# Optimization experiments

Measured on AMD Instinct MI355X. Metric: run time of the kernel, lower is better.

The kernel has to match this reference:

```python
import jax, jax.numpy as jnp
import numpy as np

NHEAD = 8
TEMP = 1.0
LAMB = 1.0
G_MIN = 1e-3


def _linear(x, w, b):
    # torch nn.Linear convention: w is (out, in)
    return x @ w.T + b


def _ln(x, s, b):
    m = x.mean(-1, keepdims=True)
    v = ((x - m) ** 2).mean(-1, keepdims=True)
    return (x - m) / jnp.sqrt(v + 1e-5) * s + b


def _gate(x, w, b):
    # UncertaintyGate, gate_mode='mu_times_evi'
    nig = _linear(x, w, b)  # [B, L, 4]
    mu = nig[..., 0]
    v = jax.nn.softplus(nig[..., 1]) + 1e-6
    alpha = jax.nn.softplus(nig[..., 2]) + 1.0 + 1e-6
    beta = jax.nn.softplus(nig[..., 3]) + 1e-6
    sigma_e2 = beta / (v * (alpha - 1.0))
    g = jax.nn.sigmoid(mu) * jnp.exp(-LAMB * sigma_e2)
    return jnp.clip(g, G_MIN, 1.0)  # [B, L]


def _cross_attn(q, k, v, gate, mask):
    B, Lq, D = q.shape
    Lk = k.shape[1]
    hd = D // NHEAD
    q = q.reshape(B, Lq, NHEAD, hd).transpose(0, 2, 1, 3)
    k = k.reshape(B, Lk, NHEAD, hd).transpose(0, 2, 1, 3)
    v = v.reshape(B, Lk, NHEAD, hd).transpose(0, 2, 1, 3)
    scores = jnp.einsum('bhqd,bhkd->bhqk', q, k) / jnp.sqrt(jnp.float32(hd))
    scores = scores + jnp.log(gate + 1e-9)[:, None, None, :]  # per-key log-gate bias
    scores = jnp.where(mask[:, None, None, :] == 0, -1e9, scores)
    attn = jax.nn.softmax(scores / TEMP, axis=-1)
    out = jnp.einsum('bhqk,bhkd->bhqd', attn, v)
    return out.transpose(0, 2, 1, 3).reshape(B, Lq, D)


def _ffn(x, w1, b1, w2, b2):
    return _linear(jax.nn.gelu(_linear(x, w1, b1), approximate=False), w2, b2)


def setup_inputs() -> dict:
    key = jax.random.key(0)
    ks = iter(jax.random.split(key, 64))
    D, B, Ld, Lp = 512, 16, 256, 1024
    def w(shape, s=0.02):
        return jax.random.normal(next(ks), shape, jnp.float32) * s
    inp = {
        'h_d': jax.random.normal(next(ks), (B, Ld, D), jnp.float32),
        'h_p': jax.random.normal(next(ks), (B, Lp, D), jnp.float32),
        'gd_w': w((4, D)), 'gd_b': jnp.zeros((4,), jnp.float32),
        'gp_w': w((4, D)), 'gp_b': jnp.zeros((4,), jnp.float32),
        'wqd_w': w((D, D)), 'wqd_b': jnp.zeros((D,), jnp.float32),
        'wkp_w': w((D, D)), 'wkp_b': jnp.zeros((D,), jnp.float32),
        'wvp_w': w((D, D)), 'wvp_b': jnp.zeros((D,), jnp.float32),
        'wqp_w': w((D, D)), 'wqp_b': jnp.zeros((D,), jnp.float32),
        'wkd_w': w((D, D)), 'wkd_b': jnp.zeros((D,), jnp.float32),
        'wvd_w': w((D, D)), 'wvd_b': jnp.zeros((D,), jnp.float32),
        'od_w': w((D, D)), 'od_b': jnp.zeros((D,), jnp.float32),
        'op_w': w((D, D)), 'op_b': jnp.zeros((D,), jnp.float32),
        'fd1_w': w((4 * D, D)), 'fd1_b': jnp.zeros((4 * D,), jnp.float32),
        'fd2_w': w((D, 4 * D)), 'fd2_b': jnp.zeros((D,), jnp.float32),
        'fp1_w': w((4 * D, D)), 'fp1_b': jnp.zeros((4 * D,), jnp.float32),
        'fp2_w': w((D, 4 * D)), 'fp2_b': jnp.zeros((D,), jnp.float32),
        'nd1_s': jnp.ones((D,), jnp.float32), 'nd1_b': jnp.zeros((D,), jnp.float32),
        'nd2_s': jnp.ones((D,), jnp.float32), 'nd2_b': jnp.zeros((D,), jnp.float32),
        'np1_s': jnp.ones((D,), jnp.float32), 'np1_b': jnp.zeros((D,), jnp.float32),
        'np2_s': jnp.ones((D,), jnp.float32), 'np2_b': jnp.zeros((D,), jnp.float32),
        'mask_d': jnp.ones((B, Ld), jnp.int32),
        'mask_p': jnp.ones((B, Lp), jnp.int32),
    }
    return inp


def reference(h_d, h_p, gd_w, gd_b, gp_w, gp_b, wqd_w, wqd_b, wkp_w, wkp_b,
              wvp_w, wvp_b, wqp_w, wqp_b, wkd_w, wkd_b, wvd_w, wvd_b,
              od_w, od_b, op_w, op_b, fd1_w, fd1_b, fd2_w, fd2_b,
              fp1_w, fp1_b, fp2_w, fp2_b, nd1_s, nd1_b, nd2_s, nd2_b,
              np1_s, np1_b, np2_s, np2_b, mask_d, mask_p):
    # gates are computed from the ORIGINAL inputs
    g_d = _gate(h_d, gd_w, gd_b)
    g_p = _gate(h_p, gp_w, gp_b)
    # drug attends to protein
    attn_d = _cross_attn(_linear(h_d, wqd_w, wqd_b),
                         _linear(h_p, wkp_w, wkp_b),
                         _linear(h_p, wvp_w, wvp_b), g_p, mask_p)
    h_d = _ln(h_d + _linear(attn_d, od_w, od_b), nd1_s, nd1_b)
    # protein attends to UPDATED drug (matches original control flow)
    attn_p = _cross_attn(_linear(h_p, wqp_w, wqp_b),
                         _linear(h_d, wkd_w, wkd_b),
                         _linear(h_d, wvd_w, wvd_b), g_d, mask_d)
    h_p = _ln(h_p + _linear(attn_p, op_w, op_b), np1_s, np1_b)
    h_d = _ln(h_d + _ffn(h_d, fd1_w, fd1_b, fd2_w, fd2_b), nd2_s, nd2_b)
    h_p = _ln(h_p + _ffn(h_p, fp1_w, fp1_b, fp2_w, fp2_b), np2_s, np2_b)
    return (h_d, h_p)
```

## Files before the change

kernel.cpp:

```cpp
#include <hip/hip_runtime.h>

typedef float f32x4 __attribute__((ext_vector_type(4)));
typedef short bfrag __attribute__((ext_vector_type(8)));
typedef short s16x8 __attribute__((ext_vector_type(8)));
typedef unsigned short u16;

__device__ __forceinline__ u16 f2bf(float f) {
  union { float f; unsigned u; } x; x.f = f;
  unsigned r = x.u + 0x7fffu + ((x.u >> 16) & 1u);
  return (u16)(r >> 16);
}
__device__ __forceinline__ float bf2f(u16 v) {
  union { unsigned u; float f; } x; x.u = ((unsigned)v) << 16;
  return x.f;
}

__device__ __forceinline__ void g2l16(const void* g, void* l) {
  void* gnc = const_cast<void*>(g);
  __builtin_amdgcn_global_load_lds((__attribute__((address_space(1))) void*)gnc,
                                   (__attribute__((address_space(3))) void*)l, 16, 0, 0);
}

__device__ __forceinline__ f32x4 mfma16(bfrag a, bfrag b, f32x4 c) {
  asm volatile("v_mfma_f32_16x16x32_bf16 %0, %1, %2, %0" : "+v"(c) : "v"(a), "v"(b));
  return c;
}

__device__ __forceinline__ float wred_sum(float s) {
  #pragma unroll
  for (int o = 32; o; o >>= 1) s += __shfl_xor(s, o);
  return s;
}

struct CvtArgs {
  const float* s[14];
  u16* d[14];
  int eb[14];
};

__global__ __launch_bounds__(256) void cvt_all(CvtArgs a) {
  const int blk = blockIdx.x;
  int base = 0;
  const float* sp = a.s[0];
  u16* dp = a.d[0];
  #pragma unroll
  for (int i = 0; i < 13; ++i) {
    if (blk >= a.eb[i]) { base = a.eb[i]; sp = a.s[i + 1]; dp = a.d[i + 1]; }
  }
  const size_t gi = ((size_t)(blk - base) * 256 + threadIdx.x) * 4;
  float4 f = *(const float4*)(sp + gi);
  ushort4 o;
  o.x = f2bf(f.x); o.y = f2bf(f.y); o.z = f2bf(f.z); o.w = f2bf(f.w);
  *(ushort4*)(dp + gi) = o;
}

__device__ __forceinline__ float softplus_s(float x) {
  return fmaxf(x, 0.f) + log1pf(expf(-fabsf(x)));
}

__global__ __launch_bounds__(256) void gate_k(
    const float* __restrict__ hd, const float* __restrict__ hp,
    const float* __restrict__ wd, const float* __restrict__ bd,
    const float* __restrict__ wp, const float* __restrict__ bp,
    float* __restrict__ lgd, float* __restrict__ lgp, int mdTok) {
  const int lane = threadIdx.x & 63, wv = threadIdx.x >> 6;
  size_t tok = (size_t)blockIdx.x * 4 + wv;
  const float* h; const float* w4; const float* b4; float* lg;
  if (tok < (size_t)mdTok) { h = hd; w4 = wd; b4 = bd; lg = lgd; }
  else { h = hp; w4 = wp; b4 = bp; lg = lgp; tok -= mdTok; }
  const float* x = h + tok * 512;
  float s0 = 0.f, s1 = 0.f, s2 = 0.f, s3 = 0.f;
  #pragma unroll
  for (int i = 0; i < 8; ++i) {
    int c = (i << 6) + lane;
    float xv = x[c];
    s0 += xv * w4[c];
    s1 += xv * w4[512 + c];
    s2 += xv * w4[1024 + c];
    s3 += xv * w4[1536 + c];
  }
  s0 = wred_sum(s0); s1 = wred_sum(s1); s2 = wred_sum(s2); s3 = wred_sum(s3);
  if (lane == 0) {
    float mu = s0 + b4[0];
    float va = softplus_s(s1 + b4[1]) + 1e-6f;
    float al = softplus_s(s2 + b4[2]) + 1.f + 1e-6f;
    float be = softplus_s(s3 + b4[3]) + 1e-6f;
    float se2 = be / (va * (al - 1.f));
    float g = (1.f / (1.f + expf(-mu))) * expf(-se2);
    g = fminf(fmaxf(g, 1e-3f), 1.f);
    lg[tok] = logf(g + 1e-9f);
  }
}

template <int RES, int OUT>
__global__ __launch_bounds__(256) void ln_k(const void* __restrict__ resv,
                                            const u16* __restrict__ y,
                                            const float* __restrict__ sc,
                                            const float* __restrict__ bi,
                                            void* __restrict__ outv) {
  const int lane = threadIdx.x & 63, w = threadIdx.x >> 6;
  const size_t row = (size_t)blockIdx.x * 4 + w;
  const int c0 = lane * 8;
  float v[8];
  s16x8 yv = *(const s16x8*)(y + row * 512 + c0);
  if constexpr (RES == 0) {
    const float* rf = (const float*)resv + row * 512 + c0;
    float4 r0 = *(const float4*)rf, r1 = *(const float4*)(rf + 4);
    v[0] = r0.x; v[1] = r0.y; v[2] = r0.z; v[3] = r0.w;
    v[4] = r1.x; v[5] = r1.y; v[6] = r1.z; v[7] = r1.w;
  } else {
    s16x8 rv = *(const s16x8*)((const u16*)resv + row * 512 + c0);
    #pragma unroll
    for (int i = 0; i < 8; ++i) v[i] = bf2f((u16)rv[i]);
  }
  float s = 0.f;
  #pragma unroll
  for (int i = 0; i < 8; ++i) { v[i] += bf2f((u16)yv[i]); s += v[i]; }
  s = wred_sum(s);
  float m = s * (1.f / 512.f);
  float s2 = 0.f;
  #pragma unroll
  for (int i = 0; i < 8; ++i) { float d = v[i] - m; s2 += d * d; }
  s2 = wred_sum(s2);
  float inv = rsqrtf(s2 * (1.f / 512.f) + 1e-5f);
  float4 sc0 = *(const float4*)(sc + c0), sc1 = *(const float4*)(sc + c0 + 4);
  float4 bi0 = *(const float4*)(bi + c0), bi1 = *(const float4*)(bi + c0 + 4);
  float scv[8] = {sc0.x, sc0.y, sc0.z, sc0.w, sc1.x, sc1.y, sc1.z, sc1.w};
  float biv[8] = {bi0.x, bi0.y, bi0.z, bi0.w, bi1.x, bi1.y, bi1.z, bi1.w};
  float o[8];
  #pragma unroll
  for (int i = 0; i < 8; ++i) o[i] = (v[i] - m) * inv * scv[i] + biv[i];
  if constexpr (OUT == 0) {
    float* of = (float*)outv + row * 512 + c0;
    *(float4*)of = float4{o[0], o[1], o[2], o[3]};
    *(float4*)(of + 4) = float4{o[4], o[5], o[6], o[7]};
  } else {
    s16x8 ov;
    #pragma unroll
    for (int i = 0; i < 8; ++i) ov[i] = (short)f2bf(o[i]);
    *(s16x8*)((u16*)outv + row * 512 + c0) = ov;
  }
}

template <int KT>
__global__ __launch_bounds__(256) void flash_k(
    const u16* __restrict__ Q, const u16* __restrict__ Kv,
    const u16* __restrict__ Vt, const float* __restrict__ logg,
    const int* __restrict__ mask, u16* __restrict__ Out,
    int Lq, int Lk, float scale) {
  __shared__ __align__(16) u16 Kl[KT * 64];
  __shared__ __align__(16) u16 Vl[64 * KT];
  __shared__ __align__(16) u16 Pl[64 * (KT + 8)];
  const int tid = threadIdx.x;
  const int lane = tid & 63, wv = tid >> 6;
  const int lr = lane & 15, lg4 = lane >> 4;
  const int bh = blockIdx.z;
  const int b = bh >> 3, h = bh & 7;
  const int q0 = blockIdx.x * 64;

  bfrag af[2];
  {
    const u16* qrow = Q + (size_t)(b * Lq + q0 + wv * 16 + lr) * 512 + h * 64;
    af[0] = *(const bfrag*)(qrow + lg4 * 8);
    af[1] = *(const bfrag*)(qrow + 32 + lg4 * 8);
  }
  float mreg[4] = {-3e38f, -3e38f, -3e38f, -3e38f};
  float lreg[4] = {0.f, 0.f, 0.f, 0.f};
  f32x4 Oa[4] = {};
  const float* lgb = logg + (size_t)b * Lk;
  const int* mkb = mask + (size_t)b * Lk;

  const int NKT = Lk / KT;
  for (int t = 0; t < NKT; ++t) {
    const int k0 = t * KT;
    __syncthreads();
    {
      const char* kb = (const char*)(Kv + (size_t)(b * Lk + k0) * 512 + h * 64);
      #pragma unroll
      for (int r = 0; r < KT / 32; ++r) {
        int o = r * 4096 + tid * 16;
        int rr = o >> 7, cd = (o >> 4) & 7;
        int cs = cd ^ (rr & 7);
        g2l16(kb + (size_t)rr * 1024 + cs * 16, (char*)Kl + o);
      }
      const char* vb = (const char*)(Vt + (size_t)bh * 64 * Lk + k0);
      #pragma unroll
      for (int r = 0; r < KT / 32; ++r) {
        int o = r * 4096 + tid * 16;
        int rr = o >> 8, cd = (o >> 4) & 15;
        int cs = (cd & 8) | ((cd & 7) ^ (rr & 7));
        g2l16(vb + (size_t)rr * (Lk * 2) + cs * 16, (char*)Vl + o);
      }
    }
    __syncthreads();

    f32x4 sa[KT / 16];
    #pragma unroll
    for (int n = 0; n < KT / 16; ++n) {
      sa[n] = f32x4{0.f, 0.f, 0.f, 0.f};
      int row = n * 16 + lr;
      #pragma unroll
      for (int ks = 0; ks < 2; ++ks) {
        bfrag kf = *(const bfrag*)(Kl + row * 64 + (((ks * 4 + lg4) ^ (row & 7)) * 8));
        sa[n] = mfma16(af[ks], kf, sa[n]);
      }
    }
    asm volatile("s_nop 7\n\ts_nop 7");

    float pv[KT / 16][4];
    float nm[4] = {-3e38f, -3e38f, -3e38f, -3e38f};
    #pragma unroll
    for (int n = 0; n < KT / 16; ++n) {
      int kk = k0 + n * 16 + lr;
      float lgv = lgb[kk];
      int mkv = mkb[kk];
      #pragma unroll
      for (int e = 0; e < 4; ++e) {
        float tv = mkv ? fmaf(sa[n][e], scale, lgv) : -1e9f;
        pv[n][e] = tv;
        nm[e] = fmaxf(nm[e], tv);
      }
    }
    float fac[4], rs[4];
    #pragma unroll
    for (int e = 0; e < 4; ++e) {
      nm[e] = fmaxf(nm[e], __shfl_xor(nm[e], 1));
      nm[e] = fmaxf(nm[e], __shfl_xor(nm[e], 2));
      nm[e] = fmaxf(nm[e], __shfl_xor(nm[e], 4));
      nm[e] = fmaxf(nm[e], __shfl_xor(nm[e], 8));
      nm[e] = fmaxf(nm[e], mreg[e]);
      fac[e] = __expf(mreg[e] - nm[e]);
      mreg[e] = nm[e];
      rs[e] = 0.f;
    }
    #pragma unroll
    for (int n = 0; n < KT / 16; ++n)
      #pragma unroll
      for (int e = 0; e < 4; ++e) {
        float p = __expf(pv[n][e] - nm[e]);
        pv[n][e] = p;
        rs[e] += p;
      }
    #pragma unroll
    for (int e = 0; e < 4; ++e) {
      rs[e] += __shfl_xor(rs[e], 1);
      rs[e] += __shfl_xor(rs[e], 2);
      rs[e] += __shfl_xor(rs[e], 4);
      rs[e] += __shfl_xor(rs[e], 8);
      lreg[e] = lreg[e] * fac[e] + rs[e];
    }
    #pragma unroll
    for (int n2 = 0; n2 < 4; ++n2)
      #pragma unroll
      for (int e = 0; e < 4; ++e) Oa[n2][e] *= fac[e];

    {
      int prow = wv * 16 + lg4 * 4;
      #pragma unroll
      for (int n = 0; n < KT / 16; ++n)
        #pragma unroll
        for (int e = 0; e < 4; ++e)
          Pl[(prow + e) * (KT + 8) + n * 16 + lr] = f2bf(pv[n][e]);
    }
    #pragma unroll
    for (int ks = 0; ks < KT / 32; ++ks) {
      bfrag pf = *(const bfrag*)(Pl + (wv * 16 + lr) * (KT + 8) + (ks * 4 + lg4) * 8);
      #pragma unroll
      for (int n2 = 0; n2 < 4; ++n2) {
        int vrow = n2 * 16 + lr;
        int ch = ks * 4 + lg4;
        int chs = (ch & 8) | ((ch & 7) ^ (vrow & 7));
        bfrag vf = *(const bfrag*)(Vl + vrow * KT + chs * 8);
        Oa[n2] = mfma16(pf, vf, Oa[n2]);
      }
    }
  }
  asm volatile("s_nop 7\n\ts_nop 7");

  float inv[4];
  #pragma unroll
  for (int e = 0; e < 4; ++e) inv[e] = 1.f / lreg[e];
  u16* ob = Out + (size_t)(b * Lq + q0 + wv * 16 + lg4 * 4) * 512 + h * 64;
  #pragma unroll
  for (int n2 = 0; n2 < 4; ++n2)
    #pragma unroll
    for (int e = 0; e < 4; ++e)
      ob[(size_t)e * 512 + n2 * 16 + lr] = f2bf(Oa[n2][e] * inv[e]);
}

template <int FM, int FN, int EPI>
__global__ __launch_bounds__(256) void gemm_k(
    const u16* __restrict__ A, const u16* __restrict__ W,
    const float* __restrict__ bias, void* __restrict__ C,
    int K, int lda, int ldw, int ldc, int NB, int TR) {
  constexpr int BM = 2 * FM * 16;
  constexpr int BN = 2 * FN * 16;
  __shared__ __align__(16) u16 Al[2][BM * 64];
  __shared__ __align__(16) u16 Wl[2][BN * 64];
  const int tid = threadIdx.x;
  const int qq = gridDim.x >> 3;
  const int wg = (blockIdx.x & 7) * qq + (blockIdx.x >> 3);
  const int bx = wg % NB, by = wg / NB;
  const int row0 = by * BM, col0 = bx * BN;
  const int lane = tid & 63, wv = tid >> 6;
  const int wr = wv >> 1, wc = wv & 1;
  const int rowW = wr * FM * 16, colW = wc * FN * 16;
  const int lr = lane & 15, lg4 = lane >> 4;

  f32x4 acc[FM][FN] = {};
  const int NT = K >> 6;

  auto stage = [&](int bsel, int k0) {
    #pragma unroll
    for (int r = 0; r < BM / 32; ++r) {
      int o = r * 4096 + tid * 16;
      int arow = o >> 7, cd = (o >> 4) & 7, cs = cd ^ (arow & 7);
      g2l16((const char*)(A + (size_t)(row0 + arow) * lda + k0) + cs * 16,
            (char*)Al[bsel] + o);
    }
    #pragma unroll
    for (int r = 0; r < BN / 32; ++r) {
      int o = r * 4096 + tid * 16;
      int wrow = o >> 7, cd = (o >> 4) & 7, cs = cd ^ (wrow & 7);
      g2l16((const char*)(W + (size_t)(col0 + wrow) * ldw + k0) + cs * 16,
            (char*)Wl[bsel] + o);
    }
  };

  stage(0, 0);
  int cur = 0;
  for (int t = 0; t < NT; ++t) {
    if (t + 1 < NT) {
      stage(cur ^ 1, (t + 1) << 6);
      asm volatile("s_waitcnt vmcnt(8)" ::: "memory");
    } else {
      asm volatile("s_waitcnt vmcnt(0)" ::: "memory");
    }
    asm volatile("s_barrier" ::: "memory");
    #pragma unroll
    for (int ks = 0; ks < 2; ++ks) {
      bfrag af[FM], wf[FN];
      #pragma unroll
      for (int m = 0; m < FM; ++m) {
        int rowi = rowW + m * 16 + lr;
        af[m] =
            *(const bfrag*)(Al[cur] + rowi * 64 + (((ks * 4 + lg4) ^ (rowi & 7)) * 8));
      }
      #pragma unroll
      for (int n = 0; n < FN; ++n) {
        int rowi = colW + n * 16 + lr;
        wf[n] =
            *(const bfrag*)(Wl[cur] + rowi * 64 + (((ks * 4 + lg4) ^ (rowi & 7)) * 8));
      }
      #pragma unroll
      for (int m = 0; m < FM; ++m)
        #pragma unroll
        for (int n = 0; n < FN; ++n) acc[m][n] = mfma16(af[m], wf[n], acc[m][n]);
    }
    asm volatile("s_barrier" ::: "memory");
    cur ^= 1;
  }
  asm volatile("s_nop 7\n\ts_nop 7\n\ts_nop 7");

  #pragma unroll
  for (int m = 0; m < FM; ++m) {
    #pragma unroll
    for (int n = 0; n < FN; ++n) {
      int rb = row0 + rowW + m * 16 + lg4 * 4;
      int c = col0 + colW + n * 16 + lr;
      float bv = bias[c];
      if constexpr (EPI == 1) {
        u16* Cu = (u16*)C;
        #pragma unroll
        for (int e = 0; e < 4; ++e)
          Cu[(size_t)(rb + e) * ldc + c] = f2bf(acc[m][n][e] + bv);
      } else if constexpr (EPI == 2) {
        u16* Cu = (u16*)C;
        #pragma unroll
        for (int e = 0; e < 4; ++e) {
          float vv = acc[m][n][e] + bv;
          float gl = 0.5f * vv * (1.f + erff(vv * 0.70710678118f));
          Cu[(size_t)(rb + e) * ldc + c] = f2bf(gl);
        }
      } else {
        u16* Cu = (u16*)C;
        int b2 = rb / TR, j0 = rb - b2 * TR;
        int h2 = c >> 6, dd = c & 63;
        ushort4 pk;
        pk.x = f2bf(acc[m][n][0] + bv);
        pk.y = f2bf(acc[m][n][1] + bv);
        pk.z = f2bf(acc[m][n][2] + bv);
        pk.w = f2bf(acc[m][n][3] + bv);
        *(ushort4*)&Cu[(((size_t)b2 * 8 + h2) * 64 + dd) * TR + j0] = pk;
      }
    }
  }
}

extern "C" void kernel_launch(void* const* d_in, const int* in_sizes, int n_in,
                              void* d_out, int out_size, void* d_ws, size_t ws_size,
                              hipStream_t stream) {
  const float* h_d = (const float*)d_in[0];
  const float* h_p = (const float*)d_in[1];
  const float* gd_w = (const float*)d_in[2];
  const float* gd_b = (const float*)d_in[3];
  const float* gp_w = (const float*)d_in[4];
  const float* gp_b = (const float*)d_in[5];
  const float* wqd_w = (const float*)d_in[6];  const float* wqd_b = (const float*)d_in[7];
  const float* wkp_w = (const float*)d_in[8];  const float* wkp_b = (const float*)d_in[9];
  const float* wvp_w = (const float*)d_in[10]; const float* wvp_b = (const float*)d_in[11];
  const float* wqp_w = (const float*)d_in[12]; const float* wqp_b = (const float*)d_in[13];
  const float* wkd_w = (const float*)d_in[14]; const float* wkd_b = (const float*)d_in[15];
  const float* wvd_w = (const float*)d_in[16]; const float* wvd_b = (const float*)d_in[17];
  const float* od_w = (const float*)d_in[18];  const float* od_b = (const float*)d_in[19];
  const float* op_w = (const float*)d_in[20];  const float* op_b = (const float*)d_in[21];
  const float* fd1_w = (const float*)d_in[22]; const float* fd1_b = (const float*)d_in[23];
  const float* fd2_w = (const float*)d_in[24]; const float* fd2_b = (const float*)d_in[25];
  const float* fp1_w = (const float*)d_in[26]; const float* fp1_b = (const float*)d_in[27];
  const float* fp2_w = (const float*)d_in[28]; const float* fp2_b = (const float*)d_in[29];
  const float* nd1_s = (const float*)d_in[30]; const float* nd1_b = (const float*)d_in[31];
  const float* nd2_s = (const float*)d_in[32]; const float* nd2_b = (const float*)d_in[33];
  const float* np1_s = (const float*)d_in[34]; const float* np1_b = (const float*)d_in[35];
  const float* np2_s = (const float*)d_in[36]; const float* np2_b = (const float*)d_in[37];
  const int* mask_d = (const int*)d_in[38];
  const int* mask_p = (const int*)d_in[39];

  constexpr int B = 16, Ld = 256, Lp = 1024, D = 512, H = 8, F = 2048;
  constexpr int Md = B * Ld;
  constexpr int Mp = B * Lp;
  constexpr int BH = B * H;

  char* ws = (char*)d_ws;
  size_t off = 0;
  auto alloc = [&](size_t bytes) {
    size_t o = off;
    off += (bytes + 255) & ~(size_t)255;
    return o;
  };
  auto a16 = [&](size_t els) { return (u16*)(ws + alloc(els * 2)); };
  auto a32 = [&](size_t els) { return (float*)(ws + alloc(els * 4)); };

  u16* w_qd = a16((size_t)D * D);
  u16* w_kp = a16((size_t)D * D);
  u16* w_vp = a16((size_t)D * D);
  u16* w_qp = a16((size_t)D * D);
  u16* w_kd = a16((size_t)D * D);
  u16* w_vd = a16((size_t)D * D);
  u16* w_od = a16((size_t)D * D);
  u16* w_op = a16((size_t)D * D);
  u16* w_fd1 = a16((size_t)F * D);
  u16* w_fd2 = a16((size_t)F * D);
  u16* w_fp1 = a16((size_t)F * D);
  u16* w_fp2 = a16((size_t)F * D);

  u16* hd16 = a16((size_t)Md * D);
  u16* hd2_16 = a16((size_t)Md * D);
  u16* hp16 = a16((size_t)Mp * D);
  u16* qd16 = a16((size_t)Md * D);
  u16* kp16 = a16((size_t)Mp * D);
  u16* vt16 = a16((size_t)Mp * D);
  u16* obuf16 = a16((size_t)Mp * D);
  u16* t16 = a16((size_t)Mp * F);
  float* logg_d = a32(Md);
  float* logg_p = a32(Mp);

  {
    CvtArgs a;
    const float* src[14] = {h_d, h_p, wqd_w, wkp_w, wvp_w, wqp_w, wkd_w,
                            wvd_w, od_w, op_w, fd1_w, fd2_w, fp1_w, fp2_w};
    u16* dst[14] = {hd16, hp16, w_qd, w_kp, w_vp, w_qp, w_kd,
                    w_vd, w_od, w_op, w_fd1, w_fd2, w_fp1, w_fp2};
    const int nelem[14] = {Md * D, Mp * D, D * D, D * D, D * D, D * D, D * D,
                           D * D, D * D, D * D, F * D, F * D, F * D, F * D};
    int pfx = 0;
    for (int i = 0; i < 14; ++i) {
      a.s[i] = src[i];
      a.d[i] = dst[i];
      pfx += nelem[i] / 1024;
      a.eb[i] = pfx;
    }
    cvt_all<<<pfx, 256, 0, stream>>>(a);
  }

  gate_k<<<(Md + Mp) / 4, 256, 0, stream>>>(h_d, h_p, gd_w, gd_b, gp_w, gp_b,
                                            logg_d, logg_p, Md);

  gemm_k<4, 4, 1><<<(Md / 128) * (D / 128), 256, 0, stream>>>(
      hd16, w_qd, wqd_b, qd16, D, D, D, D, D / 128, 0);
  gemm_k<4, 4, 1><<<(Mp / 128) * (D / 128), 256, 0, stream>>>(
      hp16, w_kp, wkp_b, kp16, D, D, D, D, D / 128, 0);
  gemm_k<4, 4, 3><<<(Mp / 128) * (D / 128), 256, 0, stream>>>(
      hp16, w_vp, wvp_b, vt16, D, D, D, 0, D / 128, Lp);

  flash_k<128><<<dim3(Ld / 64, 1, BH), 256, 0, stream>>>(
      qd16, kp16, vt16, logg_p, mask_p, hd16, Ld, Lp, 0.125f);

  gemm_k<4, 4, 1><<<(Md / 128) * (D / 128), 256, 0, stream>>>(
      hd16, w_od, od_b, obuf16, D, D, D, D, D / 128, 0);
  ln_k<0, 1><<<Md / 4, 256, 0, stream>>>(h_d, obuf16, nd1_s, nd1_b, hd2_16);

  gemm_k<4, 4, 1><<<(Mp / 128) * (D / 128), 256, 0, stream>>>(
      hp16, w_qp, wqp_b, kp16, D, D, D, D, D / 128, 0);
  gemm_k<4, 4, 1><<<(Md / 128) * (D / 128), 256, 0, stream>>>(
      hd2_16, w_kd, wkd_b, qd16, D, D, D, D, D / 128, 0);
  gemm_k<4, 4, 3><<<(Md / 128) * (D / 128), 256, 0, stream>>>(
      hd2_16, w_vd, wvd_b, vt16, D, D, D, 0, D / 128, Ld);

  flash_k<128><<<dim3(Lp / 64, 1, BH), 256, 0, stream>>>(
      kp16, qd16, vt16, logg_d, mask_d, hp16, Lp, Ld, 0.125f);

  gemm_k<4, 4, 1><<<(Mp / 128) * (D / 128), 256, 0, stream>>>(
      hp16, w_op, op_b, obuf16, D, D, D, D, D / 128, 0);
  ln_k<0, 1><<<Mp / 4, 256, 0, stream>>>(h_p, obuf16, np1_s, np1_b, hp16);

  gemm_k<4, 4, 2><<<(Md / 128) * (F / 128), 256, 0, stream>>>(
      hd2_16, w_fd1, fd1_b, t16, D, D, D, F, F / 128, 0);
  gemm_k<4, 4, 1><<<(Md / 128) * (D / 128), 256, 0, stream>>>(
      t16, w_fd2, fd2_b, obuf16, F, F, F, D, D / 128, 0);
  ln_k<1, 0><<<Md / 4, 256, 0, stream>>>(hd2_16, obuf16, nd2_s, nd2_b, (float*)d_out);

  gemm_k<4, 4, 2><<<(Mp / 128) * (F / 128), 256, 0, stream>>>(
      hp16, w_fp1, fp1_b, t16, D, D, D, F, F / 128, 0);
  gemm_k<4, 4, 1><<<(Mp / 128) * (D / 128), 256, 0, stream>>>(
      t16, w_fp2, fp2_b, obuf16, F, F, F, D, D / 128, 0);
  ln_k<1, 0><<<Mp / 4, 256, 0, stream>>>(hp16, obuf16, np2_s, np2_b,
                                         (float*)d_out + (size_t)Md * D);
}
```

Baseline: 394.5 us.

## Use single-buffered LDS in GEMM and precompute load/fragment addresses

Replaces the double-buffered LDS staging in the GEMM kernel with one buffer that is loaded, synchronized and consumed each k-step. Global source pointers and LDS fragment offsets are precomputed once before the loop. The aim is to halve LDS footprint, possibly raising occupancy, and to cut per-iteration address arithmetic. In exchange, global-load latency is no longer overlapped with MFMA compute within a block.

```diff
diff --git a/kernel.cpp b/kernel.cpp
--- a/kernel.cpp
+++ b/kernel.cpp
@@ -295,8 +295,8 @@
     int K, int lda, int ldw, int ldc, int NB, int TR) {
   constexpr int BM = 2 * FM * 16;
   constexpr int BN = 2 * FN * 16;
-  __shared__ __align__(16) u16 Al[2][BM * 64];
-  __shared__ __align__(16) u16 Wl[2][BN * 64];
+  __shared__ __align__(16) u16 Al[BM * 64];
+  __shared__ __align__(16) u16 Wl[BN * 64];
   const int tid = threadIdx.x;
   const int qq = gridDim.x >> 3;
   const int wg = (blockIdx.x & 7) * qq + (blockIdx.x >> 3);
@@ -307,58 +307,60 @@
   const int rowW = wr * FM * 16, colW = wc * FN * 16;
   const int lr = lane & 15, lg4 = lane >> 4;
 
+  const u16* aSrc[BM / 32];
+  const u16* wSrc[BN / 32];
+  int aDst[BM / 32], wDst[BN / 32];
+  #pragma unroll
+  for (int r = 0; r < BM / 32; ++r) {
+    int o = r * 4096 + tid * 16;
+    int arow = o >> 7, cd = (o >> 4) & 7, cs = cd ^ (arow & 7);
+    aSrc[r] = A + (size_t)(row0 + arow) * lda + cs * 8;
+    aDst[r] = o;
+  }
+  #pragma unroll
+  for (int r = 0; r < BN / 32; ++r) {
+    int o = r * 4096 + tid * 16;
+    int wrow = o >> 7, cd = (o >> 4) & 7, cs = cd ^ (wrow & 7);
+    wSrc[r] = W + (size_t)(col0 + wrow) * ldw + cs * 8;
+    wDst[r] = o;
+  }
+  int aOff[FM][2], wOff[FN][2];
+  #pragma unroll
+  for (int m = 0; m < FM; ++m) {
+    int rowi = rowW + m * 16 + lr;
+    #pragma unroll
+    for (int ks = 0; ks < 2; ++ks)
+      aOff[m][ks] = rowi * 64 + (((ks * 4 + lg4) ^ (rowi & 7)) * 8);
+  }
+  #pragma unroll
+  for (int n = 0; n < FN; ++n) {
+    int rowi = colW + n * 16 + lr;
+    #pragma unroll
+    for (int ks = 0; ks < 2; ++ks)
+      wOff[n][ks] = rowi * 64 + (((ks * 4 + lg4) ^ (rowi & 7)) * 8);
+  }
+
   f32x4 acc[FM][FN] = {};
-  const int NT = K >> 6;
-
-  auto stage = [&](int bsel, int k0) {
-    #pragma unroll
-    for (int r = 0; r < BM / 32; ++r) {
-      int o = r * 4096 + tid * 16;
-      int arow = o >> 7, cd = (o >> 4) & 7, cs = cd ^ (arow & 7);
-      g2l16((const char*)(A + (size_t)(row0 + arow) * lda + k0) + cs * 16,
-            (char*)Al[bsel] + o);
-    }
-    #pragma unroll
-    for (int r = 0; r < BN / 32; ++r) {
-      int o = r * 4096 + tid * 16;
-      int wrow = o >> 7, cd = (o >> 4) & 7, cs = cd ^ (wrow & 7);
-      g2l16((const char*)(W + (size_t)(col0 + wrow) * ldw + k0) + cs * 16,
-            (char*)Wl[bsel] + o);
-    }
-  };
-
-  stage(0, 0);
-  int cur = 0;
-  for (int t = 0; t < NT; ++t) {
-    if (t + 1 < NT) {
-      stage(cur ^ 1, (t + 1) << 6);
-      asm volatile("s_waitcnt vmcnt(8)" ::: "memory");
-    } else {
-      asm volatile("s_waitcnt vmcnt(0)" ::: "memory");
-    }
-    asm volatile("s_barrier" ::: "memory");
+
+  for (int k0 = 0; k0 < K; k0 += 64) {
+    #pragma unroll
+    for (int r = 0; r < BM / 32; ++r) g2l16(aSrc[r] + k0, (char*)Al + aDst[r]);
+    #pragma unroll
+    for (int r = 0; r < BN / 32; ++r) g2l16(wSrc[r] + k0, (char*)Wl + wDst[r]);
+    __syncthreads();
     #pragma unroll
     for (int ks = 0; ks < 2; ++ks) {
       bfrag af[FM], wf[FN];
       #pragma unroll
-      for (int m = 0; m < FM; ++m) {
-        int rowi = rowW + m * 16 + lr;
-        af[m] =
-            *(const bfrag*)(Al[cur] + rowi * 64 + (((ks * 4 + lg4) ^ (rowi & 7)) * 8));
-      }
-      #pragma unroll
-      for (int n = 0; n < FN; ++n) {
-        int rowi = colW + n * 16 + lr;
-        wf[n] =
-            *(const bfrag*)(Wl[cur] + rowi * 64 + (((ks * 4 + lg4) ^ (rowi & 7)) * 8));
-      }
+      for (int m = 0; m < FM; ++m) af[m] = *(const bfrag*)(Al + aOff[m][ks]);
+      #pragma unroll
+      for (int n = 0; n < FN; ++n) wf[n] = *(const bfrag*)(Wl + wOff[n][ks]);
       #pragma unroll
       for (int m = 0; m < FM; ++m)
         #pragma unroll
         for (int n = 0; n < FN; ++n) acc[m][n] = mfma16(af[m], wf[n], acc[m][n]);
     }
-    asm volatile("s_barrier" ::: "memory");
-    cur ^= 1;
+    __syncthreads();
   }
   asm volatile("s_nop 7\n\ts_nop 7\n\ts_nop 7");
 
```

Result: no change. 390.3 us (-1.1%).
